# Kernel optimization log

Hardware: AMD Instinct MI355X
Metric: run time of the kernel (lower is better)

## Reference

```python
import jax, jax.numpy as jnp
import numpy as np

B, N, D = 4, 2048, 256
ALPHA = 0.2  # LeakyReLU negative slope
NEG = -1e9


def setup_inputs() -> dict:
    key = jax.random.key(0)
    ks = jax.random.split(key, 16)
    f = lambda k, s: jax.random.normal(k, s, dtype=jnp.float32)
    sc = 0.02
    spk = jax.random.randint(ks[13], (B, N), 0, 2)
    intra_mask = (spk[:, :, None] == spk[:, None, :]).astype(jnp.int32)
    inter_mask = 1 - intra_mask
    return {
        'inp': f(ks[0], (B, N, D)),
        'emo_vector': f(ks[1], (B, N, D)),
        'event_csk_before': f(ks[2], (B, N, D)),
        'event_csk_after': f(ks[3], (B, N, D)),
        'emo_intra_csk': f(ks[4], (B, N, D)),
        'emo_inter_csk': f(ks[5], (B, N, D)),
        'int_intra_csk': f(ks[6], (B, N, D)),
        'int_inter_csk': f(ks[7], (B, N, D)),
        'W': f(ks[8], (D, D)) * sc,
        'a': f(ks[9], (2 * D,)) * sc,
        'csk_W': f(ks[10], (D, D)) * sc,
        'csk_b': jnp.zeros((D,), jnp.float32),
        'emo_lin_W': f(ks[11], (4, D, D)) * sc,  # order: weight, query, key, value
        'emo_lin_b': jnp.zeros((4, D), jnp.float32),
        'act_lin_W': f(ks[12], (4, D, D)) * sc,
        'act_lin_b': jnp.zeros((4, D), jnp.float32),
        'conv_len': jax.random.randint(ks[14], (B,), N // 2, N + 1),
        'intra_mask': intra_mask,
        'inter_mask': inter_mask,
    }


def _csk_measure(tv, hv, temo, icsk, ocsk, tim, tom, lin_W, lin_b, add_emo):
    # tv/temo: [B,1,D] target vectors; hv: [B,N,D]; tim/tom: [B,1,N] float masks
    wW, qW, kW, vW = lin_W
    wb, qb, kb, vb = lin_b
    q = (tv + temo if add_emo else tv) @ qW + qb            # [B,1,D]
    w_i = icsk @ wW + wb
    w_o = ocsk @ wW + wb
    k_base = hv @ kW + kb
    v_base = hv @ vW + vb
    k_i, v_i = k_base + w_i, v_base + w_i                   # [B,N,D]
    k_o, v_o = k_base + w_o, v_base + w_o
    inv = 1.0 / jnp.sqrt(jnp.float32(D))
    s_i = jnp.einsum('bqd,bnd->bqn', q, k_i) * inv * tim    # [B,1,N]
    s_o = jnp.einsum('bqd,bnd->bqn', q, k_o) * inv * tom
    m = tim + tom
    probs = jax.nn.softmax(jnp.where(m == 0, NEG, s_i + s_o), axis=-1)  # [B,1,N]
    p_i = (probs * tim).transpose(0, 2, 1)                  # [B,N,1]
    p_o = (probs * tom).transpose(0, 2, 1)
    target_enh = p_i * q + p_o * q                          # q broadcasts [B,1,D]->[B,N,D]
    csk_enh = p_i * v_i + p_o * v_o
    return target_enh + csk_enh, probs


def reference(inp, emo_vector, event_csk_before, event_csk_after,
              emo_intra_csk, emo_inter_csk, int_intra_csk, int_inter_csk,
              W, a, csk_W, csk_b, emo_lin_W, emo_lin_b, act_lin_W, act_lin_b,
              conv_len, intra_mask, inter_mask):
    im = intra_mask.astype(jnp.float32)
    om = inter_mask.astype(jnp.float32)
    h = inp @ W                                             # [B,N,D]
    evt = (event_csk_after @ csk_W + csk_b) + (event_csk_before @ csk_W + csk_b)
    # GAT scoring without materializing [B,N,N,2D]:
    # e[b,i,j] = leaky_relu(h[b,i].a1 + (h+evt)[b,j].a2)
    a1, a2 = a[:D], a[D:]
    s1 = h @ a1                                             # [B,N]
    s2 = (h + evt) @ a2                                     # [B,N]
    e_pair = jax.nn.leaky_relu(s1[:, :, None] + s2[:, None, :], ALPHA)  # [B,N,N]
    e = e_pair * im + e_pair * om
    adj = im + om
    attention = jax.nn.softmax(jnp.where(adj == 0, NEG, e), axis=-1)
    h_prime = jnp.einsum('bij,bjd->bid', attention, h)      # [B,N,D]
    # gather target (last utterance) per conversation
    b_idx = jnp.arange(inp.shape[0])
    t_idx = conv_len - 1
    tv = inp[b_idx, t_idx][:, None, :]                      # [B,1,D]
    temo = emo_vector[b_idx, t_idx][:, None, :]
    tim = im[b_idx, t_idx][:, None, :]                      # [B,1,N]
    tom = om[b_idx, t_idx][:, None, :]
    emo_conn, emo_probs = _csk_measure(tv, h_prime, temo, emo_intra_csk,
                                       emo_inter_csk, tim, tom,
                                       emo_lin_W, emo_lin_b, add_emo=True)
    int_conn, act_probs = _csk_measure(tv, h_prime, temo, int_intra_csk,
                                       int_inter_csk, tim, tom,
                                       act_lin_W, act_lin_b, add_emo=False)
    out = h_prime + inp + emo_conn + int_conn
    return jax.nn.relu(out), emo_probs, act_probs
```

## Files before the change

kernel.cpp:

```cpp
#include <hip/hip_runtime.h>
#include <math.h>


namespace {
constexpr int B = 4, N = 2048, D = 256;
constexpr float ALPHA = 0.2f;
constexpr float INVS  = 0.0625f;

constexpr size_t OFF_H     = 0;
constexpr size_t OFF_HP    = 2097152;
constexpr size_t OFF_UE    = 4194304;
constexpr size_t OFF_UA    = 6291456;
constexpr size_t OFF_PPOS  = 8388608;
constexpr size_t OFF_PNEG  = 10486784;
constexpr size_t OFF_S1    = 12584960;
constexpr size_t OFF_S2    = OFF_S1 + 8192;
constexpr size_t OFF_SV    = OFF_S2 + 8192;
constexpr size_t OFF_SIDX  = OFF_SV + 8192;
constexpr size_t OFF_WP    = OFF_SIDX + 8192;
constexpr size_t OFF_WN    = OFF_WP + 8192;
constexpr size_t OFF_ZP    = OFF_WN + 8192;
constexpr size_t OFF_ZN    = OFF_ZP + 8196;
constexpr size_t OFF_PARTP = OFF_ZN + 8196;
constexpr size_t OFF_PARTN = OFF_PARTP + 32768;
constexpr size_t OFF_LE    = OFF_PARTN + 32768;
constexpr size_t OFF_LA    = OFF_LE + 8192;
constexpr size_t OFF_SET   = OFF_LA + 8192;
constexpr size_t KQE = OFF_SET + 0;
constexpr size_t WQE = OFF_SET + 1024;
constexpr size_t KQA = OFF_SET + 2048;
constexpr size_t WQA = OFF_SET + 3072;
constexpr size_t QCE = OFF_SET + 4096;
constexpr size_t QCA = OFF_SET + 5120;
constexpr size_t CA2 = OFF_SET + 6144;
constexpr size_t CEc = OFF_SET + 6400;
constexpr size_t CAc = OFF_SET + 6404;
constexpr size_t C2c = OFF_SET + 6408;
constexpr size_t OFF_RNK   = OFF_SET + 8192;
constexpr size_t OFF_C0    = OFF_RNK + 8192;
constexpr size_t OFF_C1    = OFF_C0 + 8192;
constexpr size_t OFF_PARTQ = OFF_C1 + 8192;
constexpr size_t OFF_QE    = OFF_PARTQ + 32768;
constexpr size_t OFF_QA    = OFF_QE + 1024;
constexpr size_t OFF_BT    = OFF_QA + 1024;
constexpr size_t OFF_PCNT  = OFF_BT + 163840;
constexpr size_t OFF_LEU   = OFF_PCNT + 131072;
constexpr size_t OFF_LAU   = OFF_LEU + 8192;
constexpr size_t SMXE      = OFF_LAU + 8192;
constexpr size_t SIVE      = SMXE + 4;
constexpr size_t SMXA      = SIVE + 4;
constexpr size_t SIVA      = SMXA + 4;
}

typedef __attribute__((ext_vector_type(8))) short bf16x8;
typedef __attribute__((ext_vector_type(4))) float f32x4;

__device__ inline float wave_sum(float v) {
#pragma unroll
  for (int off = 32; off > 0; off >>= 1) v += __shfl_xor(v, off, 64);
  return v;
}

__device__ inline ushort f2bf(float x) {
  union { float f; uint u; } v; v.f = x;
  return (ushort)((v.u + 0x7FFFu + ((v.u >> 16) & 1u)) >> 16);
}
__device__ inline uint pk2bf(float a, float b) {
  return (uint)f2bf(a) | ((uint)f2bf(b) << 16);
}

__global__ __launch_bounds__(256) void k_btq(
    const float* __restrict__ Wm, const float* __restrict__ eW,
    const float* __restrict__ aW, const float* __restrict__ inp,
    const float* __restrict__ emo, const int* __restrict__ cl,
    ushort* __restrict__ bt, float* __restrict__ ws)
{
  __shared__ float smem[64*65];
  if (blockIdx.y < 5) {
    int m = blockIdx.y;
    const float* src = (m == 0) ? Wm : (m == 1) ? eW + 3*65536 : (m == 2) ? eW
                     : (m == 3) ? aW + 3*65536 : aW;
    ushort* dst = bt + (size_t)m*65536;
    int k0 = (blockIdx.x >> 2)*64, n0 = (blockIdx.x & 3)*64;
    int r = threadIdx.x >> 2, c0 = (threadIdx.x & 3)*16;
#pragma unroll
    for (int cc = 0; cc < 16; cc += 4)
      *(float4*)&smem[r*65 + c0+cc] = *(const float4*)&src[(size_t)(k0+r)*256 + n0 + c0 + cc];
    __syncthreads();
    int n = threadIdx.x >> 2, kq = (threadIdx.x & 3)*16;
    uint4 o0, o1;
    o0.x = pk2bf(smem[(kq+ 0)*65+n], smem[(kq+ 1)*65+n]);
    o0.y = pk2bf(smem[(kq+ 2)*65+n], smem[(kq+ 3)*65+n]);
    o0.z = pk2bf(smem[(kq+ 4)*65+n], smem[(kq+ 5)*65+n]);
    o0.w = pk2bf(smem[(kq+ 6)*65+n], smem[(kq+ 7)*65+n]);
    o1.x = pk2bf(smem[(kq+ 8)*65+n], smem[(kq+ 9)*65+n]);
    o1.y = pk2bf(smem[(kq+10)*65+n], smem[(kq+11)*65+n]);
    o1.z = pk2bf(smem[(kq+12)*65+n], smem[(kq+13)*65+n]);
    o1.w = pk2bf(smem[(kq+14)*65+n], smem[(kq+15)*65+n]);
    *(uint4*)&dst[(size_t)(n0+n)*256 + k0 + kq]     = o0;
    *(uint4*)&dst[(size_t)(n0+n)*256 + k0 + kq + 8] = o1;
  } else {
    int c = blockIdx.x;
// ... 87 lines not shown
    if (d == 0) ws[C2c] = 2.0f * red[0];
  }
}

__global__ __launch_bounds__(256) void k_rowdots(
    const float* __restrict__ eW, const float* __restrict__ aW,
    const float* __restrict__ cskW, const float* __restrict__ a,
    float* __restrict__ ws)
{
  int job = blockIdx.y;
  int wid = threadIdx.x >> 6, lane = threadIdx.x & 63;
  int row = blockIdx.x*4 + wid;
  __shared__ float vec[D];
  const float* M; size_t outo;
  if (job < 16) {
    int b = job >> 2, m = (job >> 1) & 1, which = job & 1;
    const float* base = m ? aW : eW;
    M = base + (which ? 0 : (size_t)2*D*D);
    if (threadIdx.x < D)
      vec[threadIdx.x] = ws[(m ? OFF_QA : OFF_QE) + (size_t)b*D + threadIdx.x];
    outo = (which ? (m ? WQA : WQE) : (m ? KQA : KQE)) + (size_t)b*D;
  } else {
    M = cskW;
    if (threadIdx.x < D) vec[threadIdx.x] = a[D + threadIdx.x];
    outo = CA2;
  }
  __syncthreads();
  float4 w = *reinterpret_cast<const float4*>(&M[(size_t)row*D + lane*4]);
  float s = w.x*vec[lane*4] + w.y*vec[lane*4+1] + w.z*vec[lane*4+2] + w.w*vec[lane*4+3];
  s = wave_sum(s);
  if (lane == 0) ws[outo + row] = s;
}

__global__ __launch_bounds__(256) void k_u(
    const float* __restrict__ ei, const float* __restrict__ eo,
    const float* __restrict__ ai, const float* __restrict__ ao,
    const int* __restrict__ cl, const int* __restrict__ intra,
    float* __restrict__ ws)
{
  size_t g = (size_t)blockIdx.x*256 + threadIdx.x;
  size_t base = g << 2;
  int b = (int)(base >> 19);
  int n = (int)((base >> 8) & (N - 1));
  int d0 = (int)(base & (D - 1));
  int t = cl[b] - 1;
  float tm = (float)intra[(size_t)b*N*N + (size_t)t*N + n];
  float om = 1.0f - tm;
  float4 vei = *(const float4*)&ei[base];
  float4 veo = *(const float4*)&eo[base];
  float4 vai = *(const float4*)&ai[base];
  float4 vao = *(const float4*)&ao[base];
  float4 ue, ua;
  ue.x = tm*vei.x + om*veo.x; ue.y = tm*vei.y + om*veo.y;
  ue.z = tm*vei.z + om*veo.z; ue.w = tm*vei.w + om*veo.w;
  ua.x = tm*vai.x + om*vao.x; ua.y = tm*vai.y + om*vao.y;
  ua.z = tm*vai.z + om*vao.z; ua.w = tm*vai.w + om*vao.w;
  *(float4*)&ws[OFF_UE + base] = ue;
  *(float4*)&ws[OFF_UA + base] = ua;
  float4 wqe = *(const float4*)&ws[WQE + (size_t)b*D + d0];
  float4 wqa = *(const float4*)&ws[WQA + (size_t)b*D + d0];
  float se = ue.x*wqe.x + ue.y*wqe.y + ue.z*wqe.z + ue.w*wqe.w;
  float sa = ua.x*wqa.x + ua.y*wqa.y + ua.z*wqa.z + ua.w*wqa.w;
  se = wave_sum(se); sa = wave_sum(sa);
  if ((threadIdx.x & 63) == 0) {
    size_t row = base >> 8;
    ws[OFF_LEU + row] = se;
    ws[OFF_LAU + row] = sa;
  }
}

__global__ __launch_bounds__(256) void k_s12(
    const float* __restrict__ bef, const float* __restrict__ aft,
    const float* __restrict__ a, float* __restrict__ ws)
{
  int wid  = (int)(((size_t)blockIdx.x*256 + threadIdx.x) >> 6);
  int lane = threadIdx.x & 63;
  int d0 = lane << 2;
  float4 a1 = *(const float4*)&a[d0];
  float4 a2 = *(const float4*)&a[D + d0];
  float4 cv = *(const float4*)&ws[CA2 + d0];
  float c2  = ws[C2c];
  for (int rr = 0; rr < 4; ++rr) {
    int row = wid*4 + rr;
    float4 h4 = *(const float4*)&ws[OFF_H + (size_t)row*D + d0];
    float4 b4 = *(const float4*)&bef[(size_t)row*D + d0];
    float4 f4 = *(const float4*)&aft[(size_t)row*D + d0];
    float s1 = h4.x*a1.x + h4.y*a1.y + h4.z*a1.z + h4.w*a1.w;
    float s2 = h4.x*a2.x + h4.y*a2.y + h4.z*a2.z + h4.w*a2.w
             + (b4.x+f4.x)*cv.x + (b4.y+f4.y)*cv.y
             + (b4.z+f4.z)*cv.z + (b4.w+f4.w)*cv.w;
    s1 = wave_sum(s1); s2 = wave_sum(s2);
    if (lane == 0) { ws[OFF_S1 + row] = s1; ws[OFF_S2 + row] = s2 + c2; }
  }
}

__global__ __launch_bounds__(256) void k_cnt2(float* __restrict__ ws)
{
  int jb = blockIdx.x;
  int kb = blockIdx.y;
  int b  = blockIdx.z;
  int tid = threadIdx.x;
  __shared__ float ck[128];
  if (tid < 32)
    *(float4*)&ck[tid*4] = *(const float4*)&ws[OFF_S2 + (size_t)b*N + kb*128 + tid*4];
  __syncthreads();
  int j = jb*256 + tid;
  float v = ws[OFF_S2 + (size_t)b*N + j];
  int kg = kb*128;
  int cnt = 0;
#pragma unroll
  for (int k = 0; k < 128; k += 16) {
    float4 u0 = *(const float4*)&ck[k];
    float4 u1 = *(const float4*)&ck[k+4];
    float4 u2 = *(const float4*)&ck[k+8];
    float4 u3 = *(const float4*)&ck[k+12];
    cnt += (u0.x < v) || (u0.x == v && (kg+k+ 0) < j);
    cnt += (u0.y < v) || (u0.y == v && (kg+k+ 1) < j);
    cnt += (u0.z < v) || (u0.z == v && (kg+k+ 2) < j);
    cnt += (u0.w < v) || (u0.w == v && (kg+k+ 3) < j);
    cnt += (u1.x < v) || (u1.x == v && (kg+k+ 4) < j);
    cnt += (u1.y < v) || (u1.y == v && (kg+k+ 5) < j);
    cnt += (u1.z < v) || (u1.z == v && (kg+k+ 6) < j);
    cnt += (u1.w < v) || (u1.w == v && (kg+k+ 7) < j);
    cnt += (u2.x < v) || (u2.x == v && (kg+k+ 8) < j);
    cnt += (u2.y < v) || (u2.y == v && (kg+k+ 9) < j);
    cnt += (u2.z < v) || (u2.z == v && (kg+k+10) < j);
    cnt += (u2.w < v) || (u2.w == v && (kg+k+11) < j);
    cnt += (u3.x < v) || (u3.x == v && (kg+k+12) < j);
    cnt += (u3.y < v) || (u3.y == v && (kg+k+13) < j);
    cnt += (u3.z < v) || (u3.z == v && (kg+k+14) < j);
    cnt += (u3.w < v) || (u3.w == v && (kg+k+15) < j);
  }
  ((int*)ws)[OFF_PCNT + ((size_t)(b*16 + kb))*N + j] = cnt;
}

__global__ __launch_bounds__(256) void k_cntfin(float* __restrict__ ws)
{
  int b = blockIdx.y;
  int j = blockIdx.x*256 + threadIdx.x;
  int cnt = 0;
#pragma unroll
  for (int kb = 0; kb < 16; ++kb)
    cnt += ((const int*)ws)[OFF_PCNT + ((size_t)(b*16 + kb))*N + j];
  float v = ws[OFF_S2 + (size_t)b*N + j];
  size_t o = (size_t)b*N + cnt;
  ws[OFF_SV + o] = v;
  ((int*)ws)[OFF_SIDX + o] = j;
  ws[OFF_WP + o] = expf(v);
  ws[OFF_WN + o] = expf(ALPHA*v);
}

__global__ __launch_bounds__(1024) void k_scan(float* __restrict__ ws)
{
  int b = blockIdx.x, m = blockIdx.y, t = threadIdx.x;
  const float* src = ws + (m ? OFF_WN : OFF_WP) + (size_t)b*N;
  float* dst = ws + (m ? OFF_ZN : OFF_ZP) + (size_t)b*(N+1);
  __shared__ float buf[N];
  buf[t] = src[t]; buf[t + 1024] = src[t + 1024];
  __syncthreads();
  for (int off = 1; off < N; off <<= 1) {
    float v0 = (t >= off)        ? buf[t - off]        : 0.f;
    float v1 = (t + 1024 >= off) ? buf[t + 1024 - off] : 0.f;
    __syncthreads();
    buf[t] += v0; buf[t + 1024] += v1;
    __syncthreads();
  }
  if (t == 0) dst[0] = 0.f;
  dst[t + 1]    = buf[t];
  dst[t + 1025] = buf[t + 1024];
}

__global__ __launch_bounds__(256) void k_rank(float* __restrict__ ws)
{
  int b = blockIdx.y;
  int i = blockIdx.x * 256 + threadIdx.x;
  __shared__ float sv[N];
  for (int r = threadIdx.x; r < N; r += 256) sv[r] = ws[OFF_SV + (size_t)b*N + r];
  __syncthreads();
  float s1i = ws[OFF_S1 + (size_t)b*N + i];
  float th = -s1i;
  int lo = 0, hi = N;
  while (lo < hi) { int mid = (lo + hi) >> 1; if (sv[mid] <= th) lo = mid + 1; else hi = mid; }
  int r = lo;
  float ep = expf(s1i), en = expf(ALPHA*s1i);
  float zp  = ws[OFF_ZP + (size_t)b*(N+1) + r];
  float zn  = ws[OFF_ZN + (size_t)b*(N+1) + r];
  float zpT = ws[OFF_ZP + (size_t)b*(N+1) + N];
  float den = ep*(zpT - zp) + en*zn;
  ((int*)ws)[OFF_RNK + (size_t)b*N + i] = r;
  ws[OFF_C0 + (size_t)b*N + i] = ep/den;
  ws[OFF_C1 + (size_t)b*N + i] = en/den;
}

__global__ __launch_bounds__(256) void k_p1(float* __restrict__ ws)
{
  int c = blockIdx.x, b = blockIdx.y, d = threadIdx.x;
  const int*   sidx = (const int*)ws + OFF_SIDX + (size_t)b*N;
  const float* wp = ws + OFF_WP + (size_t)b*N;
  const float* wn = ws + OFF_WN + (size_t)b*N;
  const float* h  = ws + OFF_H + (size_t)b*N*D;
  float ap = 0.f, an = 0.f;
  for (int r = c*64; r < c*64 + 64; ++r) {
    float hv = h[(size_t)sidx[r]*D + d];
    ap += wp[r]*hv; an += wn[r]*hv;
  }
  ws[OFF_PARTP + ((size_t)b*32 + c)*D + d] = ap;
  ws[OFF_PARTN + ((size_t)b*32 + c)*D + d] = an;
}

__global__ __launch_bounds__(256) void k_p3(float* __restrict__ ws)
{
  int c = blockIdx.x, b = blockIdx.y, d = threadIdx.x;
  const int*   sidx = (const int*)ws + OFF_SIDX + (size_t)b*N;
  const float* wp = ws + OFF_WP + (size_t)b*N;
  const float* wn = ws + OFF_WN + (size_t)b*N;
  const float* h  = ws + OFF_H + (size_t)b*N*D;
  float ap = 0.f, an = 0.f;
  for (int c2 = 0; c2 < c; ++c2) {
    ap += ws[OFF_PARTP + ((size_t)b*32 + c2)*D + d];
    an += ws[OFF_PARTN + ((size_t)b*32 + c2)*D + d];
  }
  for (int r = c*64; r < c*64 + 64; ++r) {
    ws[OFF_PPOS + ((size_t)b*(N+1) + r)*D + d] = ap;
    ws[OFF_PNEG + ((size_t)b*(N+1) + r)*D + d] = an;
    float hv = h[(size_t)sidx[r]*D + d];
    ap += wp[r]*hv; an += wn[r]*hv;
  }
  if (c == 31) {
    ws[OFF_PPOS + ((size_t)b*(N+1) + N)*D + d] = ap;
    ws[OFF_PNEG + ((size_t)b*(N+1) + N)*D + d] = an;
  }
}

__global__ __launch_bounds__(256) void k_hprime2(float* __restrict__ ws)
{
  int b = blockIdx.y, d = threadIdx.x;
  int i0 = blockIdx.x * 8;
  float totp = ws[OFF_PPOS + ((size_t)b*(N+1) + N)*D + d];
  float kqe = ws[KQE + (size_t)b*D + d];
  float kqa = ws[KQA + (size_t)b*D + d];
  float se[8], sa[8];
#pragma unroll
  for (int ii = 0; ii < 8; ++ii) {
    int i = i0 + ii;
    int   r  = ((const int*)ws)[OFF_RNK + (size_t)b*N + i];
    float c0 = ws[OFF_C0 + (size_t)b*N + i];
    float c1 = ws[OFF_C1 + (size_t)b*N + i];
    float pp = ws[OFF_PPOS + ((size_t)b*(N+1) + r)*D + d];
    float pn = ws[OFF_PNEG + ((size_t)b*(N+1) + r)*D + d];
    float v = c0*(totp - pp) + c1*pn;
    ws[OFF_HP + ((size_t)b*N + i)*D + d] = v;
    se[ii] = v*kqe;
    sa[ii] = v*kqa;
  }
  __shared__ float lred[16][4];
  int w = d >> 6, lane = d & 63;
#pragma unroll
  for (int ii = 0; ii < 8; ++ii) {
    float s = wave_sum(se[ii]);
    if (lane == 0) lred[ii][w] = s;
    s = wave_sum(sa[ii]);
    if (lane == 0) lred[8 + ii][w] = s;
  }
  __syncthreads();
  if (d < 16) {
    float s = lred[d][0] + lred[d][1] + lred[d][2] + lred[d][3];
    size_t row = (size_t)b*N + i0 + (d & 7);
    if (d < 8) ws[OFF_LE + row] = (s + ws[OFF_LEU + row] + ws[CEc + b]) * INVS;
    else       ws[OFF_LA + row] = (s + ws[OFF_LAU + row] + ws[CAc + b]) * INVS;
  }
}

__global__ __launch_bounds__(256) void k_smred(float* __restrict__ ws)
{
  int b = blockIdx.x, m = blockIdx.y, t = threadIdx.x;
  const float* l = ws + (m ? OFF_LA : OFF_LE) + (size_t)b*N;
  __shared__ float red[256];
  float v[8];
  float mx = -1e30f;
#pragma unroll
  for (int k = 0; k < 8; ++k) { v[k] = l[t*8 + k]; mx = fmaxf(mx, v[k]); }
  red[t] = mx; __syncthreads();
  for (int s = 128; s > 0; s >>= 1) { if (t < s) red[t] = fmaxf(red[t], red[t+s]); __syncthreads(); }
  mx = red[0]; __syncthreads();
  float sum = 0.f;
#pragma unroll
  for (int k = 0; k < 8; ++k) sum += expf(v[k] - mx);
  red[t] = sum; __syncthreads();
  for (int s = 128; s > 0; s >>= 1) { if (t < s) red[t] += red[t+s]; __syncthreads(); }
  if (t == 0) {
    ws[(m ? SMXA : SMXE) + b] = mx;
    ws[(m ? SIVA : SIVE) + b] = 1.0f / red[0];
  }
}

__global__ __launch_bounds__(256) void k_tail(
    const float* __restrict__ inp, const ushort* __restrict__ bt,
    float* __restrict__ ws, float* __restrict__ out)
{
  __shared__ ushort Hs[32*40], Es[32*40], Zs[32*40];
  __shared__ float qec[256], qac[256];
  const int t = threadIdx.x;
  const int m0 = blockIdx.x * 32, n0 = blockIdx.y * 128;
  const int b = m0 >> 11;
  const int lane = t & 63, w = t >> 6;
  const int laneN = lane & 15, kg = lane >> 4;
  qec[t] = ws[QCE + (size_t)b*D + t];
  qac[t] = ws[QCA + (size_t)b*D + t];
  const int srow = t >> 3, sc = (t & 7) * 4;
  const float* hp = ws + OFF_HP;
  const float* ue = ws + OFF_UE;
  const float* ua = ws + OFF_UA;
  const ushort* Bve = bt + 1*65536;
  const ushort* Bwe = bt + 2*65536;
  const ushort* Bva = bt + 3*65536;
  const ushort* Bwa = bt + 4*65536;
  f32x4 accE[2][2] = {}, accA[2][2] = {};
  for (int k0 = 0; k0 < 256; k0 += 32) {
    __syncthreads();
    size_t abase = (size_t)(m0 + srow)*256 + k0 + sc;
    float4 h4 = *(const float4*)&hp[abase];
    float4 e4 = *(const float4*)&ue[abase];
    float4 z4 = *(const float4*)&ua[abase];
    uint2 oh; oh.x = pk2bf(h4.x, h4.y); oh.y = pk2bf(h4.z, h4.w);
    uint2 oe; oe.x = pk2bf(e4.x, e4.y); oe.y = pk2bf(e4.z, e4.w);
    uint2 oz; oz.x = pk2bf(z4.x, z4.y); oz.y = pk2bf(z4.z, z4.w);
    *(uint2*)&Hs[srow*40 + sc] = oh;
    *(uint2*)&Es[srow*40 + sc] = oe;
    *(uint2*)&Zs[srow*40 + sc] = oz;
    __syncthreads();
    bf16x8 hf[2], ef[2], zf[2];
#pragma unroll
    for (int i = 0; i < 2; ++i) {
      hf[i] = *(const bf16x8*)&Hs[(i*16 + laneN)*40 + kg*8];
      ef[i] = *(const bf16x8*)&Es[(i*16 + laneN)*40 + kg*8];
      zf[i] = *(const bf16x8*)&Zs[(i*16 + laneN)*40 + kg*8];
    }
#pragma unroll
    for (int j = 0; j < 2; ++j) {
      size_t cb = (size_t)(n0 + w*32 + j*16 + laneN)*256 + k0 + kg*8;
      bf16x8 bve = *(const bf16x8*)&Bve[cb];
      bf16x8 bwe = *(const bf16x8*)&Bwe[cb];
      bf16x8 bva = *(const bf16x8*)&Bva[cb];
      bf16x8 bwa = *(const bf16x8*)&Bwa[cb];
#pragma unroll
      for (int i = 0; i < 2; ++i) {
        accE[i][j] = __builtin_amdgcn_mfma_f32_16x16x32_bf16(hf[i], bve, accE[i][j], 0, 0, 0);
        accE[i][j] = __builtin_amdgcn_mfma_f32_16x16x32_bf16(ef[i], bwe, accE[i][j], 0, 0, 0);
        accA[i][j] = __builtin_amdgcn_mfma_f32_16x16x32_bf16(hf[i], bva, accA[i][j], 0, 0, 0);
        accA[i][j] = __builtin_amdgcn_mfma_f32_16x16x32_bf16(zf[i], bwa, accA[i][j], 0, 0, 0);
      }
    }
  }
  float smxe = ws[SMXE + b], sive = ws[SIVE + b];
  float smxa = ws[SMXA + b], siva = ws[SIVA + b];
  if (blockIdx.y == 0 && t < 32) {
    size_t row = (size_t)m0 + t;
    int n = (int)(row & (N - 1));
    float pe = expf(ws[OFF_LE + row] - smxe) * sive;
    float pa = expf(ws[OFF_LA + row] - smxa) * siva;
    out[(size_t)B*N*D + (size_t)b*N + n] = pe;
    out[(size_t)B*N*D + (size_t)B*N + (size_t)b*N + n] = pa;
  }
#pragma unroll
  for (int i = 0; i < 2; ++i) {
#pragma unroll
    for (int r = 0; r < 4; ++r) {
      size_t row = (size_t)m0 + i*16 + kg*4 + r;
      float pe = expf(ws[OFF_LE + row] - smxe) * sive;
      float pa = expf(ws[OFF_LA + row] - smxa) * siva;
#pragma unroll
      for (int j = 0; j < 2; ++j) {
        int col = n0 + w*32 + j*16 + laneN;
        size_t idx = row*256 + col;
        float o = hp[idx] + inp[idx] + pe*(qec[col] + accE[i][j][r]) + pa*(qac[col] + accA[i][j][r]);
        out[idx] = fmaxf(o, 0.f);
      }
    }
  }
}

extern "C" void kernel_launch(void* const* d_in, const int* in_sizes, int n_in,
                              void* d_out, int out_size, void* d_ws, size_t ws_size,
                              hipStream_t stream) {
  const float* inp  = (const float*)d_in[0];
  const float* emo  = (const float*)d_in[1];
  const float* bef  = (const float*)d_in[2];
  const float* aft  = (const float*)d_in[3];
  const float* ei   = (const float*)d_in[4];
  const float* eo   = (const float*)d_in[5];
  const float* ii   = (const float*)d_in[6];
  const float* io   = (const float*)d_in[7];
  const float* W    = (const float*)d_in[8];
  const float* a    = (const float*)d_in[9];
  const float* cskW = (const float*)d_in[10];
  const float* cskb = (const float*)d_in[11];
  const float* eW   = (const float*)d_in[12];
  const float* eb   = (const float*)d_in[13];
  const float* aW   = (const float*)d_in[14];
  const float* ab   = (const float*)d_in[15];
  const int*   cl   = (const int*)d_in[16];
  const int*   intra= (const int*)d_in[17];
  float* ws  = (float*)d_ws;
  float* out = (float*)d_out;
  ushort* bt = (ushort*)(ws + OFF_BT);

  k_btq<<<dim3(16, 7), 256, 0, stream>>>(W, eW, aW, inp, emo, cl, bt, ws);
  k_mgemmh<<<dim3(256, 2), 256, 0, stream>>>(inp, bt, ws + OFF_H);
  k_qfinish<<<dim3(B, 2), 256, 0, stream>>>(eb, ab, cskb, a, ws);
  k_rowdots<<<dim3(64, 17), 256, 0, stream>>>(eW, aW, cskW, a, ws);
  k_u<<<2048, 256, 0, stream>>>(ei, eo, ii, io, cl, intra, ws);
  k_s12<<<512, 256, 0, stream>>>(bef, aft, a, ws);
  k_cnt2<<<dim3(8, 16, B), 256, 0, stream>>>(ws);
  k_cntfin<<<dim3(8, B), 256, 0, stream>>>(ws);
  k_scan<<<dim3(B, 2), 1024, 0, stream>>>(ws);
  k_rank<<<dim3(8, B), 256, 0, stream>>>(ws);
  k_p1<<<dim3(32, B), 256, 0, stream>>>(ws);
  k_p3<<<dim3(32, B), 256, 0, stream>>>(ws);
  k_hprime2<<<dim3(256, B), 256, 0, stream>>>(ws);
  k_smred<<<dim3(B, 2), 256, 0, stream>>>(ws);
  k_tail<<<dim3(256, 2), 256, 0, stream>>>(inp, bt, ws, out);
}
```

Before: 123.3 us.

## Merge small kernels and store intermediates as bf16 for tail GEMM

```diff
diff --git a/kernel.cpp b/kernel.cpp
--- a/kernel.cpp
+++ b/kernel.cpp
@@ -15,13 +15,10 @@
 constexpr size_t OFF_PNEG  = 10486784;
 constexpr size_t OFF_S1    = 12584960;
 constexpr size_t OFF_S2    = OFF_S1 + 8192;
-constexpr size_t OFF_SV    = OFF_S2 + 8192;
-constexpr size_t OFF_SIDX  = OFF_SV + 8192;
+constexpr size_t OFF_SIDX  = OFF_S2 + 8192;
 constexpr size_t OFF_WP    = OFF_SIDX + 8192;
 constexpr size_t OFF_WN    = OFF_WP + 8192;
-constexpr size_t OFF_ZP    = OFF_WN + 8192;
-constexpr size_t OFF_ZN    = OFF_ZP + 8196;
-constexpr size_t OFF_PARTP = OFF_ZN + 8196;
+constexpr size_t OFF_PARTP = OFF_WN + 8192;
 constexpr size_t OFF_PARTN = OFF_PARTP + 32768;
 constexpr size_t OFF_LE    = OFF_PARTN + 32768;
 constexpr size_t OFF_LA    = OFF_LE + 8192;
@@ -68,6 +65,10 @@
 __device__ inline uint pk2bf(float a, float b) {
   return (uint)f2bf(a) | ((uint)f2bf(b) << 16);
 }
+__device__ inline float bf2f(ushort u) {
+  union { uint u; float f; } v; v.u = (uint)u << 16;
+  return v.f;
+}
 
 __global__ __launch_bounds__(256) void k_btq(
     const float* __restrict__ Wm, const float* __restrict__ eW,
@@ -221,65 +222,66 @@
   if (lane == 0) ws[outo + row] = s;
 }
 
-__global__ __launch_bounds__(256) void k_u(
+__global__ __launch_bounds__(256) void k_us(
     const float* __restrict__ ei, const float* __restrict__ eo,
     const float* __restrict__ ai, const float* __restrict__ ao,
     const int* __restrict__ cl, const int* __restrict__ intra,
-    float* __restrict__ ws)
-{
-  size_t g = (size_t)blockIdx.x*256 + threadIdx.x;
-  size_t base = g << 2;
-  int b = (int)(base >> 19);
-  int n = (int)((base >> 8) & (N - 1));
-  int d0 = (int)(base & (D - 1));
-  int t = cl[b] - 1;
-  float tm = (float)intra[(size_t)b*N*N + (size_t)t*N + n];
-  float om = 1.0f - tm;
-  float4 vei = *(const float4*)&ei[base];
-  float4 veo = *(const float4*)&eo[base];
-  float4 vai = *(const float4*)&ai[base];
-  float4 vao = *(const float4*)&ao[base];
-  float4 ue, ua;
-  ue.x = tm*vei.x + om*veo.x; ue.y = tm*vei.y + om*veo.y;
-  ue.z = tm*vei.z + om*veo.z; ue.w = tm*vei.w + om*veo.w;
-  ua.x = tm*vai.x + om*vao.x; ua.y = tm*vai.y + om*vao.y;
-  ua.z = tm*vai.z + om*vao.z; ua.w = tm*vai.w + om*vao.w;
-  *(float4*)&ws[OFF_UE + base] = ue;
-  *(float4*)&ws[OFF_UA + base] = ua;
-  float4 wqe = *(const float4*)&ws[WQE + (size_t)b*D + d0];
-  float4 wqa = *(const float4*)&ws[WQA + (size_t)b*D + d0];
-  float se = ue.x*wqe.x + ue.y*wqe.y + ue.z*wqe.z + ue.w*wqe.w;
-  float sa = ua.x*wqa.x + ua.y*wqa.y + ua.z*wqa.z + ua.w*wqa.w;
-  se = wave_sum(se); sa = wave_sum(sa);
-  if ((threadIdx.x & 63) == 0) {
-    size_t row = base >> 8;
-    ws[OFF_LEU + row] = se;
-    ws[OFF_LAU + row] = sa;
-  }
-}
-
-__global__ __launch_bounds__(256) void k_s12(
     const float* __restrict__ bef, const float* __restrict__ aft,
-    const float* __restrict__ a, float* __restrict__ ws)
-{
-  int wid  = (int)(((size_t)blockIdx.x*256 + threadIdx.x) >> 6);
-  int lane = threadIdx.x & 63;
-  int d0 = lane << 2;
-  float4 a1 = *(const float4*)&a[d0];
-  float4 a2 = *(const float4*)&a[D + d0];
-  float4 cv = *(const float4*)&ws[CA2 + d0];
-  float c2  = ws[C2c];
-  for (int rr = 0; rr < 4; ++rr) {
-    int row = wid*4 + rr;
-    float4 h4 = *(const float4*)&ws[OFF_H + (size_t)row*D + d0];
-    float4 b4 = *(const float4*)&bef[(size_t)row*D + d0];
-    float4 f4 = *(const float4*)&aft[(size_t)row*D + d0];
-    float s1 = h4.x*a1.x + h4.y*a1.y + h4.z*a1.z + h4.w*a1.w;
-    float s2 = h4.x*a2.x + h4.y*a2.y + h4.z*a2.z + h4.w*a2.w
-             + (b4.x+f4.x)*cv.x + (b4.y+f4.y)*cv.y
-             + (b4.z+f4.z)*cv.z + (b4.w+f4.w)*cv.w;
-    s1 = wave_sum(s1); s2 = wave_sum(s2);
-    if (lane == 0) { ws[OFF_S1 + row] = s1; ws[OFF_S2 + row] = s2 + c2; }
+    const float* __restrict__ a, float* __restrict__ ws,
+    ushort* __restrict__ ueb, ushort* __restrict__ uab)
+{
+  if (blockIdx.x < 2048) {
+    size_t g = (size_t)blockIdx.x*256 + threadIdx.x;
+    size_t base = g << 2;
+    int b = (int)(base >> 19);
+    int n = (int)((base >> 8) & (N - 1));
+    int d0 = (int)(base & (D - 1));
+    int t = cl[b] - 1;
+    float tm = (float)intra[(size_t)b*N*N + (size_t)t*N + n];
+    float om = 1.0f - tm;
+    float4 vei = *(const float4*)&ei[base];
+    float4 veo = *(const float4*)&eo[base];
+    float4 vai = *(const float4*)&ai[base];
+    float4 vao = *(const float4*)&ao[base];
+    float4 ue, ua;
+    ue.x = tm*vei.x + om*veo.x; ue.y = tm*vei.y + om*veo.y;
+    ue.z = tm*vei.z + om*veo.z; ue.w = tm*vei.w + om*veo.w;
+    ua.x = tm*vai.x + om*vao.x; ua.y = tm*vai.y + om*vao.y;
+    ua.z = tm*vai.z + om*vao.z; ua.w = tm*vai.w + om*vao.w;
+    uint2 pe; pe.x = pk2bf(ue.x, ue.y); pe.y = pk2bf(ue.z, ue.w);
+    uint2 pa; pa.x = pk2bf(ua.x, ua.y); pa.y = pk2bf(ua.z, ua.w);
+    *(uint2*)&ueb[base] = pe;
+    *(uint2*)&uab[base] = pa;
+    float4 wqe = *(const float4*)&ws[WQE + (size_t)b*D + d0];
+    float4 wqa = *(const float4*)&ws[WQA + (size_t)b*D + d0];
+    float se = ue.x*wqe.x + ue.y*wqe.y + ue.z*wqe.z + ue.w*wqe.w;
+    float sa = ua.x*wqa.x + ua.y*wqa.y + ua.z*wqa.z + ua.w*wqa.w;
+    se = wave_sum(se); sa = wave_sum(sa);
+    if ((threadIdx.x & 63) == 0) {
+      size_t row = base >> 8;
+      ws[OFF_LEU + row] = se;
+      ws[OFF_LAU + row] = sa;
+    }
+  } else {
+    int wid  = (int)(((size_t)(blockIdx.x - 2048)*256 + threadIdx.x) >> 6);
+    int lane = threadIdx.x & 63;
+    int d0 = lane << 2;
+    float4 a1 = *(const float4*)&a[d0];
+    float4 a2 = *(const float4*)&a[D + d0];
+    float4 cv = *(const float4*)&ws[CA2 + d0];
+    float c2  = ws[C2c];
+    for (int rr = 0; rr < 4; ++rr) {
+      int row = wid*4 + rr;
+      float4 h4 = *(const float4*)&ws[OFF_H + (size_t)row*D + d0];
+      float4 b4 = *(const float4*)&bef[(size_t)row*D + d0];
+      float4 f4 = *(const float4*)&aft[(size_t)row*D + d0];
+      float s1 = h4.x*a1.x + h4.y*a1.y + h4.z*a1.z + h4.w*a1.w;
+      float s2 = h4.x*a2.x + h4.y*a2.y + h4.z*a2.z + h4.w*a2.w
+               + (b4.x+f4.x)*cv.x + (b4.y+f4.y)*cv.y
+               + (b4.z+f4.z)*cv.z + (b4.w+f4.w)*cv.w;
+      s1 = wave_sum(s1); s2 = wave_sum(s2);
+      if (lane == 0) { ws[OFF_S1 + row] = s1; ws[OFF_S2 + row] = s2 + c2; }
+    }
   }
 }
 
@@ -323,62 +325,75 @@
   ((int*)ws)[OFF_PCNT + ((size_t)(b*16 + kb))*N + j] = cnt;
 }
 
-__global__ __launch_bounds__(256) void k_cntfin(float* __restrict__ ws)
-{
-  int b = blockIdx.y;
-  int j = blockIdx.x*256 + threadIdx.x;
-  int cnt = 0;
-#pragma unroll
-  for (int kb = 0; kb < 16; ++kb)
-    cnt += ((const int*)ws)[OFF_PCNT + ((size_t)(b*16 + kb))*N + j];
-  float v = ws[OFF_S2 + (size_t)b*N + j];
-  size_t o = (size_t)b*N + cnt;
-  ws[OFF_SV + o] = v;
-  ((int*)ws)[OFF_SIDX + o] = j;
-  ws[OFF_WP + o] = expf(v);
-  ws[OFF_WN + o] = expf(ALPHA*v);
-}
-
-__global__ __launch_bounds__(1024) void k_scan(float* __restrict__ ws)
-{
-  int b = blockIdx.x, m = blockIdx.y, t = threadIdx.x;
-  const float* src = ws + (m ? OFF_WN : OFF_WP) + (size_t)b*N;
-  float* dst = ws + (m ? OFF_ZN : OFF_ZP) + (size_t)b*(N+1);
-  __shared__ float buf[N];
-  buf[t] = src[t]; buf[t + 1024] = src[t + 1024];
+__global__ __launch_bounds__(1024) void k_csr(float* __restrict__ ws)
+{
+  int b = blockIdx.x, t = threadIdx.x;
+  __shared__ float sv[N];
+  __shared__ int   sx[N];
+  __shared__ float zp[N+1], zn[N+1], tmp[N];
+  const int* pc = (const int*)ws + OFF_PCNT;
+#pragma unroll
+  for (int h = 0; h < 2; ++h) {
+    int j = t + h*1024;
+    int cnt = 0;
+#pragma unroll
+    for (int kb = 0; kb < 16; ++kb)
+      cnt += pc[((size_t)(b*16 + kb))*N + j];
+    float v = ws[OFF_S2 + (size_t)b*N + j];
+    sv[cnt] = v; sx[cnt] = j;
+  }
+  __syncthreads();
+#pragma unroll
+  for (int h = 0; h < 2; ++h) {
+    int r = t + h*1024;
+    ((int*)ws)[OFF_SIDX + (size_t)b*N + r] = sx[r];
+    float w = expf(sv[r]);
+    ws[OFF_WP + (size_t)b*N + r] = w;
+    tmp[r] = w;
+  }
   __syncthreads();
   for (int off = 1; off < N; off <<= 1) {
-    float v0 = (t >= off)        ? buf[t - off]        : 0.f;
-    float v1 = (t + 1024 >= off) ? buf[t + 1024 - off] : 0.f;
-    __syncthreads();
-    buf[t] += v0; buf[t + 1024] += v1;
-    __syncthreads();
-  }
-  if (t == 0) dst[0] = 0.f;
-  dst[t + 1]    = buf[t];
-  dst[t + 1025] = buf[t + 1024];
-}
-
-__global__ __launch_bounds__(256) void k_rank(float* __restrict__ ws)
-{
-  int b = blockIdx.y;
-  int i = blockIdx.x * 256 + threadIdx.x;
-  __shared__ float sv[N];
-  for (int r = threadIdx.x; r < N; r += 256) sv[r] = ws[OFF_SV + (size_t)b*N + r];
-  __syncthreads();
-  float s1i = ws[OFF_S1 + (size_t)b*N + i];
-  float th = -s1i;
-  int lo = 0, hi = N;
-  while (lo < hi) { int mid = (lo + hi) >> 1; if (sv[mid] <= th) lo = mid + 1; else hi = mid; }
-  int r = lo;
-  float ep = expf(s1i), en = expf(ALPHA*s1i);
-  float zp  = ws[OFF_ZP + (size_t)b*(N+1) + r];
-  float zn  = ws[OFF_ZN + (size_t)b*(N+1) + r];
-  float zpT = ws[OFF_ZP + (size_t)b*(N+1) + N];
-  float den = ep*(zpT - zp) + en*zn;
-  ((int*)ws)[OFF_RNK + (size_t)b*N + i] = r;
-  ws[OFF_C0 + (size_t)b*N + i] = ep/den;
-  ws[OFF_C1 + (size_t)b*N + i] = en/den;
+    float v0 = (t >= off)        ? tmp[t - off]        : 0.f;
+    float v1 = (t + 1024 >= off) ? tmp[t + 1024 - off] : 0.f;
+    __syncthreads();
+    tmp[t] += v0; tmp[t + 1024] += v1;
+    __syncthreads();
+  }
+  if (t == 0) zp[0] = 0.f;
+  zp[t + 1] = tmp[t]; zp[t + 1025] = tmp[t + 1024];
+  __syncthreads();
+#pragma unroll
+  for (int h = 0; h < 2; ++h) {
+    int r = t + h*1024;
+    float w = expf(ALPHA*sv[r]);
+    ws[OFF_WN + (size_t)b*N + r] = w;
+    tmp[r] = w;
+  }
+  __syncthreads();
+  for (int off = 1; off < N; off <<= 1) {
+    float v0 = (t >= off)        ? tmp[t - off]        : 0.f;
+    float v1 = (t + 1024 >= off) ? tmp[t + 1024 - off] : 0.f;
+    __syncthreads();
+    tmp[t] += v0; tmp[t + 1024] += v1;
+    __syncthreads();
+  }
+  if (t == 0) zn[0] = 0.f;
+  zn[t + 1] = tmp[t]; zn[t + 1025] = tmp[t + 1024];
+  __syncthreads();
+  float zpT = zp[N];
+#pragma unroll
+  for (int h = 0; h < 2; ++h) {
+    int i = t + h*1024;
+    float s1i = ws[OFF_S1 + (size_t)b*N + i];
+    float th = -s1i;
+    int lo = 0, hi = N;
+    while (lo < hi) { int mid = (lo + hi) >> 1; if (sv[mid] <= th) lo = mid + 1; else hi = mid; }
+    float ep = expf(s1i), en = expf(ALPHA*s1i);
+    float den = ep*(zpT - zp[lo]) + en*zn[lo];
+    ((int*)ws)[OFF_RNK + (size_t)b*N + i] = lo;
+    ws[OFF_C0 + (size_t)b*N + i] = ep/den;
+    ws[OFF_C1 + (size_t)b*N + i] = en/den;
+  }
 }
 
 __global__ __launch_bounds__(256) void k_p1(float* __restrict__ ws)
@@ -421,7 +436,8 @@
   }
 }
 
-__global__ __launch_bounds__(256) void k_hprime2(float* __restrict__ ws)
+__global__ __launch_bounds__(256) void k_hprime2(float* __restrict__ ws,
+                                                 ushort* __restrict__ hpb)
 {
   int b = blockIdx.y, d = threadIdx.x;
   int i0 = blockIdx.x * 8;
@@ -438,7 +454,7 @@
     float pp = ws[OFF_PPOS + ((size_t)b*(N+1) + r)*D + d];
     float pn = ws[OFF_PNEG + ((size_t)b*(N+1) + r)*D + d];
     float v = c0*(totp - pp) + c1*pn;
-    ws[OFF_HP + ((size_t)b*N + i)*D + d] = v;
+    hpb[((size_t)b*N + i)*D + d] = f2bf(v);
     se[ii] = v*kqe;
     sa[ii] = v*kqa;
   }
@@ -485,9 +501,10 @@
 
 __global__ __launch_bounds__(256) void k_tail(
     const float* __restrict__ inp, const ushort* __restrict__ bt,
-    float* __restrict__ ws, float* __restrict__ out)
-{
-  __shared__ ushort Hs[32*40], Es[32*40], Zs[32*40];
+    float* __restrict__ ws, float* __restrict__ out,
+    const ushort* __restrict__ hpb, const ushort* __restrict__ ueb,
+    const ushort* __restrict__ uab)
+{
   __shared__ float qec[256], qac[256];
   const int t = threadIdx.x;
   const int m0 = blockIdx.x * 32, n0 = blockIdx.y * 128;
@@ -496,48 +513,34 @@
   const int laneN = lane & 15, kg = lane >> 4;
   qec[t] = ws[QCE + (size_t)b*D + t];
   qac[t] = ws[QCA + (size_t)b*D + t];
-  const int srow = t >> 3, sc = (t & 7) * 4;
-  const float* hp = ws + OFF_HP;
-  const float* ue = ws + OFF_UE;
-  const float* ua = ws + OFF_UA;
+  __syncthreads();
   const ushort* Bve = bt + 1*65536;
   const ushort* Bwe = bt + 2*65536;
   const ushort* Bva = bt + 3*65536;
   const ushort* Bwa = bt + 4*65536;
   f32x4 accE[2][2] = {}, accA[2][2] = {};
   for (int k0 = 0; k0 < 256; k0 += 32) {
-    __syncthreads();
-    size_t abase = (size_t)(m0 + srow)*256 + k0 + sc;
-    float4 h4 = *(const float4*)&hp[abase];
-    float4 e4 = *(const float4*)&ue[abase];
-    float4 z4 = *(const float4*)&ua[abase];
-    uint2 oh; oh.x = pk2bf(h4.x, h4.y); oh.y = pk2bf(h4.z, h4.w);
-    uint2 oe; oe.x = pk2bf(e4.x, e4.y); oe.y = pk2bf(e4.z, e4.w);
-    uint2 oz; oz.x = pk2bf(z4.x, z4.y); oz.y = pk2bf(z4.z, z4.w);
-    *(uint2*)&Hs[srow*40 + sc] = oh;
-    *(uint2*)&Es[srow*40 + sc] = oe;
-    *(uint2*)&Zs[srow*40 + sc] = oz;
-    __syncthreads();
-    bf16x8 hf[2], ef[2], zf[2];
-#pragma unroll
-    for (int i = 0; i < 2; ++i) {
-      hf[i] = *(const bf16x8*)&Hs[(i*16 + laneN)*40 + kg*8];
-      ef[i] = *(const bf16x8*)&Es[(i*16 + laneN)*40 + kg*8];
-      zf[i] = *(const bf16x8*)&Zs[(i*16 + laneN)*40 + kg*8];
-    }
+    bf16x8 bve[2], bwe[2], bva[2], bwa[2];
 #pragma unroll
     for (int j = 0; j < 2; ++j) {
       size_t cb = (size_t)(n0 + w*32 + j*16 + laneN)*256 + k0 + kg*8;
-      bf16x8 bve = *(const bf16x8*)&Bve[cb];
-      bf16x8 bwe = *(const bf16x8*)&Bwe[cb];
-      bf16x8 bva = *(const bf16x8*)&Bva[cb];
-      bf16x8 bwa = *(const bf16x8*)&Bwa[cb];
-#pragma unroll
-      for (int i = 0; i < 2; ++i) {
-        accE[i][j] = __builtin_amdgcn_mfma_f32_16x16x32_bf16(hf[i], bve, accE[i][j], 0, 0, 0);
-        accE[i][j] = __builtin_amdgcn_mfma_f32_16x16x32_bf16(ef[i], bwe, accE[i][j], 0, 0, 0);
-        accA[i][j] = __builtin_amdgcn_mfma_f32_16x16x32_bf16(hf[i], bva, accA[i][j], 0, 0, 0);
-        accA[i][j] = __builtin_amdgcn_mfma_f32_16x16x32_bf16(zf[i], bwa, accA[i][j], 0, 0, 0);
+      bve[j] = *(const bf16x8*)&Bve[cb];
+      bwe[j] = *(const bf16x8*)&Bwe[cb];
+      bva[j] = *(const bf16x8*)&Bva[cb];
+      bwa[j] = *(const bf16x8*)&Bwa[cb];
+    }
+#pragma unroll
+    for (int i = 0; i < 2; ++i) {
+      size_t ab = (size_t)(m0 + i*16 + laneN)*256 + k0 + kg*8;
+      bf16x8 hf = *(const bf16x8*)&hpb[ab];
+      bf16x8 ef = *(const bf16x8*)&ueb[ab];
+      bf16x8 zf = *(const bf16x8*)&uab[ab];
+#pragma unroll
+      for (int j = 0; j < 2; ++j) {
+        accE[i][j] = __builtin_amdgcn_mfma_f32_16x16x32_bf16(hf, bve[j], accE[i][j], 0, 0, 0);
+        accE[i][j] = __builtin_amdgcn_mfma_f32_16x16x32_bf16(ef, bwe[j], accE[i][j], 0, 0, 0);
+        accA[i][j] = __builtin_amdgcn_mfma_f32_16x16x32_bf16(hf, bva[j], accA[i][j], 0, 0, 0);
+        accA[i][j] = __builtin_amdgcn_mfma_f32_16x16x32_bf16(zf, bwa[j], accA[i][j], 0, 0, 0);
       }
     }
   }
@@ -562,7 +565,8 @@
       for (int j = 0; j < 2; ++j) {
         int col = n0 + w*32 + j*16 + laneN;
         size_t idx = row*256 + col;
-        float o = hp[idx] + inp[idx] + pe*(qec[col] + accE[i][j][r]) + pa*(qac[col] + accA[i][j][r]);
+        float hpv = bf2f(hpb[idx]);
+        float o = hpv + inp[idx] + pe*(qec[col] + accE[i][j][r]) + pa*(qac[col] + accA[i][j][r]);
         out[idx] = fmaxf(o, 0.f);
       }
     }
@@ -592,21 +596,21 @@
   const int*   intra= (const int*)d_in[17];
   float* ws  = (float*)d_ws;
   float* out = (float*)d_out;
-  ushort* bt = (ushort*)(ws + OFF_BT);
+  ushort* bt  = (ushort*)(ws + OFF_BT);
+  ushort* hpb = (ushort*)(ws + OFF_HP);
+  ushort* ueb = (ushort*)(ws + OFF_UE);
+  ushort* uab = (ushort*)(ws + OFF_UA);
 
   k_btq<<<dim3(16, 7), 256, 0, stream>>>(W, eW, aW, inp, emo, cl, bt, ws);
   k_mgemmh<<<dim3(256, 2), 256, 0, stream>>>(inp, bt, ws + OFF_H);
   k_qfinish<<<dim3(B, 2), 256, 0, stream>>>(eb, ab, cskb, a, ws);
   k_rowdots<<<dim3(64, 17), 256, 0, stream>>>(eW, aW, cskW, a, ws);
-  k_u<<<2048, 256, 0, stream>>>(ei, eo, ii, io, cl, intra, ws);
-  k_s12<<<512, 256, 0, stream>>>(bef, aft, a, ws);
+  k_us<<<2560, 256, 0, stream>>>(ei, eo, ii, io, cl, intra, bef, aft, a, ws, ueb, uab);
   k_cnt2<<<dim3(8, 16, B), 256, 0, stream>>>(ws);
-  k_cntfin<<<dim3(8, B), 256, 0, stream>>>(ws);
-  k_scan<<<dim3(B, 2), 1024, 0, stream>>>(ws);
-  k_rank<<<dim3(8, B), 256, 0, stream>>>(ws);
+  k_csr<<<B, 1024, 0, stream>>>(ws);
   k_p1<<<dim3(32, B), 256, 0, stream>>>(ws);
   k_p3<<<dim3(32, B), 256, 0, stream>>>(ws);
-  k_hprime2<<<dim3(256, B), 256, 0, stream>>>(ws);
+  k_hprime2<<<dim3(256, B), 256, 0, stream>>>(ws, hpb);
   k_smred<<<dim3(B, 2), 256, 0, stream>>>(ws);
-  k_tail<<<dim3(256, 2), 256, 0, stream>>>(inp, bt, ws, out);
-}
+  k_tail<<<dim3(256, 2), 256, 0, stream>>>(inp, bt, ws, out, hpb, ueb, uab);
+}
```

New measurement: 125.2 us. No clear change (+1.6%).

## Store h', ue, ua intermediates as bf16 and fuse u/s12 kernels

Applied to the files above, without the earlier changes.

```diff
diff --git a/kernel.cpp b/kernel.cpp
--- a/kernel.cpp
+++ b/kernel.cpp
@@ -68,6 +68,10 @@
 __device__ inline uint pk2bf(float a, float b) {
   return (uint)f2bf(a) | ((uint)f2bf(b) << 16);
 }
+__device__ inline float bf2f(ushort u) {
+  union { uint u; float f; } v; v.u = (uint)u << 16;
+  return v.f;
+}
 
 __global__ __launch_bounds__(256) void k_btq(
     const float* __restrict__ Wm, const float* __restrict__ eW,
@@ -221,65 +225,66 @@
   if (lane == 0) ws[outo + row] = s;
 }
 
-__global__ __launch_bounds__(256) void k_u(
+__global__ __launch_bounds__(256) void k_us(
     const float* __restrict__ ei, const float* __restrict__ eo,
     const float* __restrict__ ai, const float* __restrict__ ao,
     const int* __restrict__ cl, const int* __restrict__ intra,
-    float* __restrict__ ws)
-{
-  size_t g = (size_t)blockIdx.x*256 + threadIdx.x;
-  size_t base = g << 2;
-  int b = (int)(base >> 19);
-  int n = (int)((base >> 8) & (N - 1));
-  int d0 = (int)(base & (D - 1));
-  int t = cl[b] - 1;
-  float tm = (float)intra[(size_t)b*N*N + (size_t)t*N + n];
-  float om = 1.0f - tm;
-  float4 vei = *(const float4*)&ei[base];
-  float4 veo = *(const float4*)&eo[base];
-  float4 vai = *(const float4*)&ai[base];
-  float4 vao = *(const float4*)&ao[base];
-  float4 ue, ua;
-  ue.x = tm*vei.x + om*veo.x; ue.y = tm*vei.y + om*veo.y;
-  ue.z = tm*vei.z + om*veo.z; ue.w = tm*vei.w + om*veo.w;
-  ua.x = tm*vai.x + om*vao.x; ua.y = tm*vai.y + om*vao.y;
-  ua.z = tm*vai.z + om*vao.z; ua.w = tm*vai.w + om*vao.w;
-  *(float4*)&ws[OFF_UE + base] = ue;
-  *(float4*)&ws[OFF_UA + base] = ua;
-  float4 wqe = *(const float4*)&ws[WQE + (size_t)b*D + d0];
-  float4 wqa = *(const float4*)&ws[WQA + (size_t)b*D + d0];
-  float se = ue.x*wqe.x + ue.y*wqe.y + ue.z*wqe.z + ue.w*wqe.w;
-  float sa = ua.x*wqa.x + ua.y*wqa.y + ua.z*wqa.z + ua.w*wqa.w;
-  se = wave_sum(se); sa = wave_sum(sa);
-  if ((threadIdx.x & 63) == 0) {
-    size_t row = base >> 8;
-    ws[OFF_LEU + row] = se;
-    ws[OFF_LAU + row] = sa;
-  }
-}
-
-__global__ __launch_bounds__(256) void k_s12(
     const float* __restrict__ bef, const float* __restrict__ aft,
-    const float* __restrict__ a, float* __restrict__ ws)
-{
-  int wid  = (int)(((size_t)blockIdx.x*256 + threadIdx.x) >> 6);
-  int lane = threadIdx.x & 63;
-  int d0 = lane << 2;
-  float4 a1 = *(const float4*)&a[d0];
-  float4 a2 = *(const float4*)&a[D + d0];
-  float4 cv = *(const float4*)&ws[CA2 + d0];
-  float c2  = ws[C2c];
-  for (int rr = 0; rr < 4; ++rr) {
-    int row = wid*4 + rr;
-    float4 h4 = *(const float4*)&ws[OFF_H + (size_t)row*D + d0];
-    float4 b4 = *(const float4*)&bef[(size_t)row*D + d0];
-    float4 f4 = *(const float4*)&aft[(size_t)row*D + d0];
-    float s1 = h4.x*a1.x + h4.y*a1.y + h4.z*a1.z + h4.w*a1.w;
-    float s2 = h4.x*a2.x + h4.y*a2.y + h4.z*a2.z + h4.w*a2.w
-             + (b4.x+f4.x)*cv.x + (b4.y+f4.y)*cv.y
-             + (b4.z+f4.z)*cv.z + (b4.w+f4.w)*cv.w;
-    s1 = wave_sum(s1); s2 = wave_sum(s2);
-    if (lane == 0) { ws[OFF_S1 + row] = s1; ws[OFF_S2 + row] = s2 + c2; }
+    const float* __restrict__ a, float* __restrict__ ws,
+    ushort* __restrict__ ueb, ushort* __restrict__ uab)
+{
+  if (blockIdx.x < 2048) {
+    size_t g = (size_t)blockIdx.x*256 + threadIdx.x;
+    size_t base = g << 2;
+    int b = (int)(base >> 19);
+    int n = (int)((base >> 8) & (N - 1));
+    int d0 = (int)(base & (D - 1));
+    int t = cl[b] - 1;
+    float tm = (float)intra[(size_t)b*N*N + (size_t)t*N + n];
+    float om = 1.0f - tm;
+    float4 vei = *(const float4*)&ei[base];
+    float4 veo = *(const float4*)&eo[base];
+    float4 vai = *(const float4*)&ai[base];
+    float4 vao = *(const float4*)&ao[base];
+    float4 ue, ua;
+    ue.x = tm*vei.x + om*veo.x; ue.y = tm*vei.y + om*veo.y;
+    ue.z = tm*vei.z + om*veo.z; ue.w = tm*vei.w + om*veo.w;
+    ua.x = tm*vai.x + om*vao.x; ua.y = tm*vai.y + om*vao.y;
+    ua.z = tm*vai.z + om*vao.z; ua.w = tm*vai.w + om*vao.w;
+    uint2 pe; pe.x = pk2bf(ue.x, ue.y); pe.y = pk2bf(ue.z, ue.w);
+    uint2 pa; pa.x = pk2bf(ua.x, ua.y); pa.y = pk2bf(ua.z, ua.w);
+    *(uint2*)&ueb[base] = pe;
+    *(uint2*)&uab[base] = pa;
+    float4 wqe = *(const float4*)&ws[WQE + (size_t)b*D + d0];
+    float4 wqa = *(const float4*)&ws[WQA + (size_t)b*D + d0];
+    float se = ue.x*wqe.x + ue.y*wqe.y + ue.z*wqe.z + ue.w*wqe.w;
+    float sa = ua.x*wqa.x + ua.y*wqa.y + ua.z*wqa.z + ua.w*wqa.w;
+    se = wave_sum(se); sa = wave_sum(sa);
+    if ((threadIdx.x & 63) == 0) {
+      size_t row = base >> 8;
+      ws[OFF_LEU + row] = se;
+      ws[OFF_LAU + row] = sa;
+    }
+  } else {
+    int wid  = (int)(((size_t)(blockIdx.x - 2048)*256 + threadIdx.x) >> 6);
+    int lane = threadIdx.x & 63;
+    int d0 = lane << 2;
+    float4 a1 = *(const float4*)&a[d0];
+    float4 a2 = *(const float4*)&a[D + d0];
+    float4 cv = *(const float4*)&ws[CA2 + d0];
+    float c2  = ws[C2c];
+    for (int rr = 0; rr < 4; ++rr) {
+      int row = wid*4 + rr;
+      float4 h4 = *(const float4*)&ws[OFF_H + (size_t)row*D + d0];
+      float4 b4 = *(const float4*)&bef[(size_t)row*D + d0];
+      float4 f4 = *(const float4*)&aft[(size_t)row*D + d0];
+      float s1 = h4.x*a1.x + h4.y*a1.y + h4.z*a1.z + h4.w*a1.w;
+      float s2 = h4.x*a2.x + h4.y*a2.y + h4.z*a2.z + h4.w*a2.w
+               + (b4.x+f4.x)*cv.x + (b4.y+f4.y)*cv.y
+               + (b4.z+f4.z)*cv.z + (b4.w+f4.w)*cv.w;
+      s1 = wave_sum(s1); s2 = wave_sum(s2);
+      if (lane == 0) { ws[OFF_S1 + row] = s1; ws[OFF_S2 + row] = s2 + c2; }
+    }
   }
 }
 
@@ -421,7 +426,8 @@
   }
 }
 
-__global__ __launch_bounds__(256) void k_hprime2(float* __restrict__ ws)
+__global__ __launch_bounds__(256) void k_hprime2(float* __restrict__ ws,
+                                                 ushort* __restrict__ hpb)
 {
   int b = blockIdx.y, d = threadIdx.x;
   int i0 = blockIdx.x * 8;
@@ -438,7 +444,7 @@
     float pp = ws[OFF_PPOS + ((size_t)b*(N+1) + r)*D + d];
     float pn = ws[OFF_PNEG + ((size_t)b*(N+1) + r)*D + d];
     float v = c0*(totp - pp) + c1*pn;
-    ws[OFF_HP + ((size_t)b*N + i)*D + d] = v;
+    hpb[((size_t)b*N + i)*D + d] = f2bf(v);
     se[ii] = v*kqe;
     sa[ii] = v*kqa;
   }
@@ -485,9 +491,10 @@
 
 __global__ __launch_bounds__(256) void k_tail(
     const float* __restrict__ inp, const ushort* __restrict__ bt,
-    float* __restrict__ ws, float* __restrict__ out)
-{
-  __shared__ ushort Hs[32*40], Es[32*40], Zs[32*40];
+    float* __restrict__ ws, float* __restrict__ out,
+    const ushort* __restrict__ hpb, const ushort* __restrict__ ueb,
+    const ushort* __restrict__ uab)
+{
   __shared__ float qec[256], qac[256];
   const int t = threadIdx.x;
   const int m0 = blockIdx.x * 32, n0 = blockIdx.y * 128;
@@ -496,48 +503,34 @@
   const int laneN = lane & 15, kg = lane >> 4;
   qec[t] = ws[QCE + (size_t)b*D + t];
   qac[t] = ws[QCA + (size_t)b*D + t];
-  const int srow = t >> 3, sc = (t & 7) * 4;
-  const float* hp = ws + OFF_HP;
-  const float* ue = ws + OFF_UE;
-  const float* ua = ws + OFF_UA;
+  __syncthreads();
   const ushort* Bve = bt + 1*65536;
   const ushort* Bwe = bt + 2*65536;
   const ushort* Bva = bt + 3*65536;
   const ushort* Bwa = bt + 4*65536;
   f32x4 accE[2][2] = {}, accA[2][2] = {};
   for (int k0 = 0; k0 < 256; k0 += 32) {
-    __syncthreads();
-    size_t abase = (size_t)(m0 + srow)*256 + k0 + sc;
-    float4 h4 = *(const float4*)&hp[abase];
-    float4 e4 = *(const float4*)&ue[abase];
-    float4 z4 = *(const float4*)&ua[abase];
-    uint2 oh; oh.x = pk2bf(h4.x, h4.y); oh.y = pk2bf(h4.z, h4.w);
-    uint2 oe; oe.x = pk2bf(e4.x, e4.y); oe.y = pk2bf(e4.z, e4.w);
-    uint2 oz; oz.x = pk2bf(z4.x, z4.y); oz.y = pk2bf(z4.z, z4.w);
-    *(uint2*)&Hs[srow*40 + sc] = oh;
-    *(uint2*)&Es[srow*40 + sc] = oe;
-    *(uint2*)&Zs[srow*40 + sc] = oz;
-    __syncthreads();
-    bf16x8 hf[2], ef[2], zf[2];
-#pragma unroll
-    for (int i = 0; i < 2; ++i) {
-      hf[i] = *(const bf16x8*)&Hs[(i*16 + laneN)*40 + kg*8];
-      ef[i] = *(const bf16x8*)&Es[(i*16 + laneN)*40 + kg*8];
-      zf[i] = *(const bf16x8*)&Zs[(i*16 + laneN)*40 + kg*8];
-    }
+    bf16x8 bve[2], bwe[2], bva[2], bwa[2];
 #pragma unroll
     for (int j = 0; j < 2; ++j) {
       size_t cb = (size_t)(n0 + w*32 + j*16 + laneN)*256 + k0 + kg*8;
-      bf16x8 bve = *(const bf16x8*)&Bve[cb];
-      bf16x8 bwe = *(const bf16x8*)&Bwe[cb];
-      bf16x8 bva = *(const bf16x8*)&Bva[cb];
-      bf16x8 bwa = *(const bf16x8*)&Bwa[cb];
-#pragma unroll
-      for (int i = 0; i < 2; ++i) {
-        accE[i][j] = __builtin_amdgcn_mfma_f32_16x16x32_bf16(hf[i], bve, accE[i][j], 0, 0, 0);
-        accE[i][j] = __builtin_amdgcn_mfma_f32_16x16x32_bf16(ef[i], bwe, accE[i][j], 0, 0, 0);
-        accA[i][j] = __builtin_amdgcn_mfma_f32_16x16x32_bf16(hf[i], bva, accA[i][j], 0, 0, 0);
-        accA[i][j] = __builtin_amdgcn_mfma_f32_16x16x32_bf16(zf[i], bwa, accA[i][j], 0, 0, 0);
+      bve[j] = *(const bf16x8*)&Bve[cb];
+      bwe[j] = *(const bf16x8*)&Bwe[cb];
+      bva[j] = *(const bf16x8*)&Bva[cb];
+      bwa[j] = *(const bf16x8*)&Bwa[cb];
+    }
+#pragma unroll
+    for (int i = 0; i < 2; ++i) {
+      size_t ab = (size_t)(m0 + i*16 + laneN)*256 + k0 + kg*8;
+      bf16x8 hf = *(const bf16x8*)&hpb[ab];
+      bf16x8 ef = *(const bf16x8*)&ueb[ab];
+      bf16x8 zf = *(const bf16x8*)&uab[ab];
+#pragma unroll
+      for (int j = 0; j < 2; ++j) {
+        accE[i][j] = __builtin_amdgcn_mfma_f32_16x16x32_bf16(hf, bve[j], accE[i][j], 0, 0, 0);
+        accE[i][j] = __builtin_amdgcn_mfma_f32_16x16x32_bf16(ef, bwe[j], accE[i][j], 0, 0, 0);
+        accA[i][j] = __builtin_amdgcn_mfma_f32_16x16x32_bf16(hf, bva[j], accA[i][j], 0, 0, 0);
+        accA[i][j] = __builtin_amdgcn_mfma_f32_16x16x32_bf16(zf, bwa[j], accA[i][j], 0, 0, 0);
       }
     }
   }
@@ -562,7 +555,8 @@
       for (int j = 0; j < 2; ++j) {
         int col = n0 + w*32 + j*16 + laneN;
         size_t idx = row*256 + col;
-        float o = hp[idx] + inp[idx] + pe*(qec[col] + accE[i][j][r]) + pa*(qac[col] + accA[i][j][r]);
+        float hpv = bf2f(hpb[idx]);
+        float o = hpv + inp[idx] + pe*(qec[col] + accE[i][j][r]) + pa*(qac[col] + accA[i][j][r]);
         out[idx] = fmaxf(o, 0.f);
       }
     }
@@ -592,21 +586,23 @@
   const int*   intra= (const int*)d_in[17];
   float* ws  = (float*)d_ws;
   float* out = (float*)d_out;
-  ushort* bt = (ushort*)(ws + OFF_BT);
+  ushort* bt  = (ushort*)(ws + OFF_BT);
+  ushort* hpb = (ushort*)(ws + OFF_HP);
+  ushort* ueb = (ushort*)(ws + OFF_UE);
+  ushort* uab = (ushort*)(ws + OFF_UA);
 
   k_btq<<<dim3(16, 7), 256, 0, stream>>>(W, eW, aW, inp, emo, cl, bt, ws);
   k_mgemmh<<<dim3(256, 2), 256, 0, stream>>>(inp, bt, ws + OFF_H);
   k_qfinish<<<dim3(B, 2), 256, 0, stream>>>(eb, ab, cskb, a, ws);
   k_rowdots<<<dim3(64, 17), 256, 0, stream>>>(eW, aW, cskW, a, ws);
-  k_u<<<2048, 256, 0, stream>>>(ei, eo, ii, io, cl, intra, ws);
-  k_s12<<<512, 256, 0, stream>>>(bef, aft, a, ws);
+  k_us<<<2560, 256, 0, stream>>>(ei, eo, ii, io, cl, intra, bef, aft, a, ws, ueb, uab);
   k_cnt2<<<dim3(8, 16, B), 256, 0, stream>>>(ws);
   k_cntfin<<<dim3(8, B), 256, 0, stream>>>(ws);
   k_scan<<<dim3(B, 2), 1024, 0, stream>>>(ws);
   k_rank<<<dim3(8, B), 256, 0, stream>>>(ws);
   k_p1<<<dim3(32, B), 256, 0, stream>>>(ws);
   k_p3<<<dim3(32, B), 256, 0, stream>>>(ws);
-  k_hprime2<<<dim3(256, B), 256, 0, stream>>>(ws);
+  k_hprime2<<<dim3(256, B), 256, 0, stream>>>(ws, hpb);
   k_smred<<<dim3(B, 2), 256, 0, stream>>>(ws);
-  k_tail<<<dim3(256, 2), 256, 0, stream>>>(inp, bt, ws, out);
-}
+  k_tail<<<dim3(256, 2), 256, 0, stream>>>(inp, bt, ws, out, hpb, ueb, uab);
+}
```

Measured after the change: 127.2 us. +3.2%, slower.
